# Kernel tuning notes

Hardware: AMD Instinct MI355X
Metric: run time of the kernel (lower is better)

## Reference

```python
import jax, jax.numpy as jnp
import numpy as np

REWARD_SCALE = 1.0
DIST_NORM = 2
LATENT_DIST_THRESHOLD = 6.0

BS, N_VIEWS, N_PART, F_DIM = 128, 4, 1024, 10


def setup_inputs() -> dict:
    key = jax.random.key(0)
    k1, k2, k3, k4 = jax.random.split(key, 4)
    achieved_goal = jax.random.normal(k1, (BS, N_VIEWS, N_PART, F_DIM), jnp.float32)
    desired_goal = jax.random.normal(k2, (BS, N_VIEWS, N_PART, F_DIM), jnp.float32)
    norm_mean = jax.random.normal(k3, (F_DIM,), jnp.float32)
    norm_std = jax.random.uniform(k4, (F_DIM,), jnp.float32, minval=0.5, maxval=1.5)
    return {"achieved_goal": achieved_goal, "desired_goal": desired_goal,
            "norm_mean": norm_mean, "norm_std": norm_std}


def _pairwise_sqdist(x, y):
    # x: [bs, n, d], y: [bs, m, d] -> [bs, n, m] squared L2 ('l2_simple')
    xx = jnp.sum(x * x, axis=-1)            # [bs, n]
    yy = jnp.sum(y * y, axis=-1)            # [bs, m]
    xy = jnp.einsum('bnd,bmd->bnm', x, y)   # [bs, n, m]
    return xx[:, :, None] + yy[:, None, :] - 2.0 * xy


def _particle_mask(particles):
    # latent_classifier is None -> obj_class_cond = ones -> mask = (1 == 0) = all False
    obj_on = particles[..., -1]
    return jnp.zeros_like(obj_on, dtype=bool)


def reference(achieved_goal, desired_goal, norm_mean, norm_std):
    # unnormalize (particle_normalizer.unnormalize modeled as affine)
    state_particles = achieved_goal * norm_std + norm_mean
    goal_particles = desired_goal * norm_std + norm_mean
    bs, n_views, n_particles, _ = state_particles.shape

    state_mask = _particle_mask(state_particles)   # [bs, nv, np] bool
    goal_mask = _particle_mask(goal_particles)

    # P_mask[b,v,i,j] = state_mask[b,v,i] | goal_mask[b,v,j]
    P_mask = jnp.logical_or(state_mask[..., :, None], goal_mask[..., None, :])

    state_vis = state_particles[..., 5:9]
    state_xy = state_particles[..., :2]
    goal_vis = goal_particles[..., 5:9]
    goal_xy = goal_particles[..., :2]

    inf = jnp.asarray(jnp.inf, state_particles.dtype)
    rewards = []
    for i in range(n_views):
        sxy = state_xy[:, i]                 # [bs, np, 2]
        gxy = goal_xy[:, i]
        gmask_i = goal_mask[:, i]            # [bs, np]
        smask_i = state_mask[:, i]

        P = _pairwise_sqdist(state_vis[:, i], goal_vis[:, i])  # [bs, np_state, np_goal]
        P = jnp.where(P_mask[:, i], inf, P)

        # goal -> state direction: min over state dim (axis 1)
        min_d1 = jnp.min(P, axis=1)                            # [bs, np_goal]
        idx1 = jnp.argmin(P, axis=1)                           # [bs, np_goal]
        d_goal = jnp.take_along_axis(sxy, idx1[..., None], axis=1)  # [bs, np_goal, 2]
        xy_dist_1 = jnp.linalg.norm(gxy - d_goal, ord=DIST_NORM, axis=-1)
        xy_dist_1 = jnp.where(min_d1 > LATENT_DIST_THRESHOLD, 1.0, xy_dist_1)
        xy_dist_1 = jnp.where(gmask_i, 0.0, xy_dist_1)
        n_obj_g = jnp.maximum(jnp.sum(~gmask_i, axis=1), 1)
        reward_g2s = -jnp.sum(xy_dist_1, axis=1) / n_obj_g

        # state -> goal direction: min over goal dim (axis 2)
        min_d2 = jnp.min(P, axis=2)
        idx2 = jnp.argmin(P, axis=2)
        d_state = jnp.take_along_axis(gxy, idx2[..., None], axis=1)
        xy_dist_2 = jnp.linalg.norm(sxy - d_state, ord=DIST_NORM, axis=-1)
        xy_dist_2 = jnp.where(min_d2 > LATENT_DIST_THRESHOLD, 1.0, xy_dist_2)
        xy_dist_2 = jnp.where(smask_i, 0.0, xy_dist_2)
        n_obj_s = jnp.maximum(jnp.sum(~smask_i, axis=1), 1)
        reward_s2g = -jnp.sum(xy_dist_2, axis=1) / n_obj_s

        rv = (reward_g2s + reward_s2g) / 2.0
        no_valid = jnp.logical_or(jnp.all(gmask_i, axis=-1), jnp.all(smask_i, axis=-1))
        rv = jnp.where(no_valid, -1.0, rv)
        rewards.append(rv)

    reward = jnp.mean(jnp.stack(rewards, axis=0), axis=0)   # [bs]
    return REWARD_SCALE * reward[:, None]                    # [bs, 1]
```

## Files before the change

kernel.cpp:

```cpp
#include <hip/hip_runtime.h>
#include <cstdint>
#include <cstddef>

#define NP  1024
#define FD  10
#define NV  4
#define BSZ 128
#define TPB 128
#define RPT 8

typedef float v2f __attribute__((ext_vector_type(2)));
typedef float v4f __attribute__((ext_vector_type(4)));

extern "C" __global__ __launch_bounds__(TPB, 2)
void chamfer_pairs(const float* __restrict__ ag, const float* __restrict__ dg,
                   const float* __restrict__ nmean, const float* __restrict__ nstd,
                   float* __restrict__ out )
{
    __shared__ float cxF[NP], cyF[NP], czF[NP], cwF[NP], csF[NP];
    __shared__ float red[TPB / 64];

    const int bid  = blockIdx.x;
    const int pair = bid >> 1;
    const int d    = bid & 1;
    const int tid  = threadIdx.x;

    const float* rowsrc = ((d == 0) ? ag : dg) + (size_t)pair * (NP * FD);
    const float* colsrc = ((d == 0) ? dg : ag) + (size_t)pair * (NP * FD);

    const float s5 = -2.0f * nstd[5], m5 = -2.0f * nmean[5];
    const float s6 = -2.0f * nstd[6], m6 = -2.0f * nmean[6];
    const float s7 = -2.0f * nstd[7], m7 = -2.0f * nmean[7];
    const float s8 = -2.0f * nstd[8], m8 = -2.0f * nmean[8];
    const float std0 = nstd[0], mean0 = nmean[0];
    const float std1 = nstd[1], mean1 = nmean[1];

    for (int m = tid; m < NP; m += TPB) {
        const float* p = colsrc + (size_t)m * FD;
        float t0 = fmaf(p[5], s5, m5);
        float t1 = fmaf(p[6], s6, m6);
        float t2 = fmaf(p[7], s7, m7);
        float t3 = fmaf(p[8], s8, m8);
        cxF[m] = t0; cyF[m] = t1; czF[m] = t2; cwF[m] = t3;
        csF[m] = 0.25f * (t0 * t0 + t1 * t1 + t2 * t2 + t3 * t3);
    }

    float4 rv[RPT];
    float  rthr[RPT];
    float  bestd[RPT];
    int    bblk[RPT];
#pragma unroll
    for (int r = 0; r < RPT; ++r) {
        int n = tid + TPB * r;
        const float* p = rowsrc + (size_t)n * FD;
        float t0 = fmaf(p[5], s5, m5);
        float t1 = fmaf(p[6], s6, m6);
        float t2 = fmaf(p[7], s7, m7);
        float t3 = fmaf(p[8], s8, m8);
        rv[r] = make_float4(-0.5f * t0, -0.5f * t1, -0.5f * t2, -0.5f * t3);
        float rss = 0.25f * (t0 * t0 + t1 * t1 + t2 * t2 + t3 * t3);
        rthr[r] = 6.0f - rss;
        bestd[r] = 3.0e38f;
        bblk[r]  = 0;
    }
    __syncthreads();

    const v4f* X4 = (const v4f*)cxF;
    const v4f* Y4 = (const v4f*)cyF;
    const v4f* Z4 = (const v4f*)czF;
    const v4f* W4 = (const v4f*)cwF;
    const v4f* S4 = (const v4f*)csF;

#pragma unroll 2
    for (int g = 0; g < NP / 8; ++g) {
        const int m = g * 8;
        v4f xA = X4[2 * g], xB = X4[2 * g + 1];
        v4f yA = Y4[2 * g], yB = Y4[2 * g + 1];
        v4f zA = Z4[2 * g], zB = Z4[2 * g + 1];
        v4f wA = W4[2 * g], wB = W4[2 * g + 1];
        v4f cA = S4[2 * g], cB = S4[2 * g + 1];
#pragma unroll
        for (int r = 0; r < RPT; ++r) {
            v2f vx = {rv[r].x, rv[r].x};
            v2f vy = {rv[r].y, rv[r].y};
            v2f vz = {rv[r].z, rv[r].z};
            v2f vw = {rv[r].w, rv[r].w};
            v2f q0 = __builtin_elementwise_fma(vx, xA.lo, cA.lo);
            q0 = __builtin_elementwise_fma(vy, yA.lo, q0);
            q0 = __builtin_elementwise_fma(vz, zA.lo, q0);
            q0 = __builtin_elementwise_fma(vw, wA.lo, q0);
            v2f q1 = __builtin_elementwise_fma(vx, xA.hi, cA.hi);
            q1 = __builtin_elementwise_fma(vy, yA.hi, q1);
            q1 = __builtin_elementwise_fma(vz, zA.hi, q1);
            q1 = __builtin_elementwise_fma(vw, wA.hi, q1);
            v2f q2 = __builtin_elementwise_fma(vx, xB.lo, cB.lo);
            q2 = __builtin_elementwise_fma(vy, yB.lo, q2);
            q2 = __builtin_elementwise_fma(vz, zB.lo, q2);
            q2 = __builtin_elementwise_fma(vw, wB.lo, q2);
            v2f q3 = __builtin_elementwise_fma(vx, xB.hi, cB.hi);
            q3 = __builtin_elementwise_fma(vy, yB.hi, q3);
            q3 = __builtin_elementwise_fma(vz, zB.hi, q3);
            q3 = __builtin_elementwise_fma(vw, wB.hi, q3);
            v2f m01 = __builtin_elementwise_min(q0, q1);
            v2f m23 = __builtin_elementwise_min(q2, q3);
            v2f mm  = __builtin_elementwise_min(m01, m23);
            float bm = fminf(mm.x, mm.y);
            bool lt = bm < bestd[r];
            bestd[r] = fminf(bestd[r], bm);
            bblk[r]  = lt ? m : bblk[r];
        }
    }

    float sum = 0.0f;
#pragma unroll
    for (int r = 0; r < RPT; ++r) {
        int n  = tid + TPB * r;
        int mb = bblk[r];
        float4 v = rv[r];
        float dd[8];
#pragma unroll
        for (int j = 0; j < 8; ++j) {
            float t = fmaf(v.x, cxF[mb + j], csF[mb + j]);
            t = fmaf(v.y, cyF[mb + j], t);
            t = fmaf(v.z, czF[mb + j], t);
            t = fmaf(v.w, cwF[mb + j], t);
            dd[j] = t;
        }
        int sel = 0;
#pragma unroll
        for (int j = 7; j >= 0; --j)
            if (dd[j] == bestd[r]) sel = j;
        int idx = mb + sel;

        float gx = fmaf(colsrc[(size_t)idx * FD + 0], std0, mean0);
        float gy = fmaf(colsrc[(size_t)idx * FD + 1], std1, mean1);
        float ax = fmaf(rowsrc[(size_t)n * FD + 0], std0, mean0);
        float ay = fmaf(rowsrc[(size_t)n * FD + 1], std1, mean1);
        float dx = ax - gx;
        float dy = ay - gy;
        float dist = sqrtf(dx * dx + dy * dy);
        if (bestd[r] > rthr[r]) dist = 1.0f;
        sum += dist;
    }

    for (int o = 32; o > 0; o >>= 1) sum += __shfl_down(sum, o, 64);
    if ((tid & 63) == 0) red[tid >> 6] = sum;
    __syncthreads();
    if (tid == 0) {
        float s = red[0] + red[1];
        atomicAdd(&out[pair >> 2], s * (-1.0f / 8192.0f));
    }
}

extern "C" void kernel_launch(void* const* d_in, const int* in_sizes, int n_in,
                              void* d_out, int out_size, void* d_ws, size_t ws_size,
                              hipStream_t stream)
{
    const float* ag = (const float*)d_in[0];
    const float* dg = (const float*)d_in[1];
    const float* nm = (const float*)d_in[2];
    const float* ns = (const float*)d_in[3];

    hipMemsetAsync(d_out, 0, BSZ * sizeof(float), stream);
    chamfer_pairs<<<BSZ * NV * 2, TPB, 0, stream>>>(ag, dg, nm, ns, (float*)d_out);
}
```

Baseline: 228.2 us.

## Use single-wave blocks with 16 rows per thread and op_sel packed FMAs

Each block is now one 64-thread wave, and each thread handles 16 rows instead of 8. Every shared-memory candidate load is therefore reused across twice as many rows. The inner distance loop uses inline v_pk_fma_f32 with op_sel to broadcast row components, removing the per-row broadcast vector construction. The cross-wave LDS reduction and barrier are dropped, and the argmin refinement recomputes candidate features from global memory. The risk is fewer waves per SIMD to hide latency, plus higher register pressure.

```diff
diff --git a/kernel.cpp b/kernel.cpp
--- a/kernel.cpp
+++ b/kernel.cpp
@@ -4,21 +4,38 @@
 
 #define NP  1024
 #define FD  10
-#define NV  4
 #define BSZ 128
-#define TPB 128
-#define RPT 8
+#define TPB 64
+#define RPT 16
 
 typedef float v2f __attribute__((ext_vector_type(2)));
 typedef float v4f __attribute__((ext_vector_type(4)));
 
-extern "C" __global__ __launch_bounds__(TPB, 2)
+#define SHUF2(v, a, b) __builtin_shufflevector((v), (v), (a), (b))
+
+static __device__ __forceinline__ v2f pk_fma_lo(v2f a, v2f b, v2f c) {
+    v2f d;
+    asm("v_pk_fma_f32 %0, %1, %2, %3 op_sel:[0,0,0] op_sel_hi:[0,1,1]"
+        : "=v"(d) : "v"(a), "v"(b), "v"(c));
+    return d;
+}
+static __device__ __forceinline__ v2f pk_fma_hi(v2f a, v2f b, v2f c) {
+    v2f d;
+    asm("v_pk_fma_f32 %0, %1, %2, %3 op_sel:[1,0,0] op_sel_hi:[1,1,1]"
+        : "=v"(d) : "v"(a), "v"(b), "v"(c));
+    return d;
+}
+
+extern "C" __global__ __launch_bounds__(TPB)
 void chamfer_pairs(const float* __restrict__ ag, const float* __restrict__ dg,
                    const float* __restrict__ nmean, const float* __restrict__ nstd,
                    float* __restrict__ out )
 {
-    __shared__ float cxF[NP], cyF[NP], czF[NP], cwF[NP], csF[NP];
-    __shared__ float red[TPB / 64];
+    __shared__ __align__(16) float cxF[NP];
+    __shared__ __align__(16) float cyF[NP];
+    __shared__ __align__(16) float czF[NP];
+    __shared__ __align__(16) float cwF[NP];
+    __shared__ __align__(16) float csF[NP];
 
     const int bid  = blockIdx.x;
     const int pair = bid >> 1;
@@ -32,6 +49,10 @@
     const float s6 = -2.0f * nstd[6], m6 = -2.0f * nmean[6];
     const float s7 = -2.0f * nstd[7], m7 = -2.0f * nmean[7];
     const float s8 = -2.0f * nstd[8], m8 = -2.0f * nmean[8];
+    const float p5 = nstd[5], q5 = nmean[5];
+    const float p6 = nstd[6], q6 = nmean[6];
+    const float p7 = nstd[7], q7 = nmean[7];
+    const float p8 = nstd[8], q8 = nmean[8];
     const float std0 = nstd[0], mean0 = nmean[0];
     const float std1 = nstd[1], mean1 = nmean[1];
 
@@ -45,21 +66,20 @@
         csF[m] = 0.25f * (t0 * t0 + t1 * t1 + t2 * t2 + t3 * t3);
     }
 
-    float4 rv[RPT];
-    float  rthr[RPT];
-    float  bestd[RPT];
-    int    bblk[RPT];
+    v2f  rxy[RPT];
+    v2f  rzw[RPT];
+    float bestd[RPT];
+    int   bblk[RPT];
 #pragma unroll
     for (int r = 0; r < RPT; ++r) {
         int n = tid + TPB * r;
         const float* p = rowsrc + (size_t)n * FD;
-        float t0 = fmaf(p[5], s5, m5);
-        float t1 = fmaf(p[6], s6, m6);
-        float t2 = fmaf(p[7], s7, m7);
-        float t3 = fmaf(p[8], s8, m8);
-        rv[r] = make_float4(-0.5f * t0, -0.5f * t1, -0.5f * t2, -0.5f * t3);
-        float rss = 0.25f * (t0 * t0 + t1 * t1 + t2 * t2 + t3 * t3);
-        rthr[r] = 6.0f - rss;
+        float a0 = fmaf(p[5], p5, q5);
+        float a1 = fmaf(p[6], p6, q6);
+        float a2 = fmaf(p[7], p7, q7);
+        float a3 = fmaf(p[8], p8, q8);
+        rxy[r].x = a0; rxy[r].y = a1;
+        rzw[r].x = a2; rzw[r].y = a3;
         bestd[r] = 3.0e38f;
         bblk[r]  = 0;
     }
@@ -71,7 +91,6 @@
     const v4f* W4 = (const v4f*)cwF;
     const v4f* S4 = (const v4f*)csF;
 
-#pragma unroll 2
     for (int g = 0; g < NP / 8; ++g) {
         const int m = g * 8;
         v4f xA = X4[2 * g], xB = X4[2 * g + 1];
@@ -79,32 +98,31 @@
         v4f zA = Z4[2 * g], zB = Z4[2 * g + 1];
         v4f wA = W4[2 * g], wB = W4[2 * g + 1];
         v4f cA = S4[2 * g], cB = S4[2 * g + 1];
+        v2f x0 = SHUF2(xA, 0, 1), x1 = SHUF2(xA, 2, 3), x2 = SHUF2(xB, 0, 1), x3 = SHUF2(xB, 2, 3);
+        v2f y0 = SHUF2(yA, 0, 1), y1 = SHUF2(yA, 2, 3), y2 = SHUF2(yB, 0, 1), y3 = SHUF2(yB, 2, 3);
+        v2f z0 = SHUF2(zA, 0, 1), z1 = SHUF2(zA, 2, 3), z2 = SHUF2(zB, 0, 1), z3 = SHUF2(zB, 2, 3);
+        v2f w0 = SHUF2(wA, 0, 1), w1 = SHUF2(wA, 2, 3), w2 = SHUF2(wB, 0, 1), w3 = SHUF2(wB, 2, 3);
+        v2f c0 = SHUF2(cA, 0, 1), c1 = SHUF2(cA, 2, 3), c2 = SHUF2(cB, 0, 1), c3 = SHUF2(cB, 2, 3);
 #pragma unroll
         for (int r = 0; r < RPT; ++r) {
-            v2f vx = {rv[r].x, rv[r].x};
-            v2f vy = {rv[r].y, rv[r].y};
-            v2f vz = {rv[r].z, rv[r].z};
-            v2f vw = {rv[r].w, rv[r].w};
-            v2f q0 = __builtin_elementwise_fma(vx, xA.lo, cA.lo);
-            q0 = __builtin_elementwise_fma(vy, yA.lo, q0);
-            q0 = __builtin_elementwise_fma(vz, zA.lo, q0);
-            q0 = __builtin_elementwise_fma(vw, wA.lo, q0);
-            v2f q1 = __builtin_elementwise_fma(vx, xA.hi, cA.hi);
-            q1 = __builtin_elementwise_fma(vy, yA.hi, q1);
-            q1 = __builtin_elementwise_fma(vz, zA.hi, q1);
-            q1 = __builtin_elementwise_fma(vw, wA.hi, q1);
-            v2f q2 = __builtin_elementwise_fma(vx, xB.lo, cB.lo);
-            q2 = __builtin_elementwise_fma(vy, yB.lo, q2);
-            q2 = __builtin_elementwise_fma(vz, zB.lo, q2);
-            q2 = __builtin_elementwise_fma(vw, wB.lo, q2);
-            v2f q3 = __builtin_elementwise_fma(vx, xB.hi, cB.hi);
-            q3 = __builtin_elementwise_fma(vy, yB.hi, q3);
-            q3 = __builtin_elementwise_fma(vz, zB.hi, q3);
-            q3 = __builtin_elementwise_fma(vw, wB.hi, q3);
-            v2f m01 = __builtin_elementwise_min(q0, q1);
-            v2f m23 = __builtin_elementwise_min(q2, q3);
-            v2f mm  = __builtin_elementwise_min(m01, m23);
-            float bm = fminf(mm.x, mm.y);
+            v2f u0 = pk_fma_lo(rxy[r], x0, c0);
+            u0 = pk_fma_hi(rxy[r], y0, u0);
+            u0 = pk_fma_lo(rzw[r], z0, u0);
+            u0 = pk_fma_hi(rzw[r], w0, u0);
+            v2f u1 = pk_fma_lo(rxy[r], x1, c1);
+            u1 = pk_fma_hi(rxy[r], y1, u1);
+            u1 = pk_fma_lo(rzw[r], z1, u1);
+            u1 = pk_fma_hi(rzw[r], w1, u1);
+            v2f u2 = pk_fma_lo(rxy[r], x2, c2);
+            u2 = pk_fma_hi(rxy[r], y2, u2);
+            u2 = pk_fma_lo(rzw[r], z2, u2);
+            u2 = pk_fma_hi(rzw[r], w2, u2);
+            v2f u3 = pk_fma_lo(rxy[r], x3, c3);
+            u3 = pk_fma_hi(rxy[r], y3, u3);
+            u3 = pk_fma_lo(rzw[r], z3, u3);
+            u3 = pk_fma_hi(rzw[r], w3, u3);
+            float bm = fminf(fminf(fminf(u0.x, u0.y), fminf(u1.x, u1.y)),
+                             fminf(fminf(u2.x, u2.y), fminf(u3.x, u3.y)));
             bool lt = bm < bestd[r];
             bestd[r] = fminf(bestd[r], bm);
             bblk[r]  = lt ? m : bblk[r];
@@ -116,14 +134,20 @@
     for (int r = 0; r < RPT; ++r) {
         int n  = tid + TPB * r;
         int mb = bblk[r];
-        float4 v = rv[r];
+        float vx = rxy[r].x, vy = rxy[r].y, vz = rzw[r].x, vw = rzw[r].y;
         float dd[8];
 #pragma unroll
         for (int j = 0; j < 8; ++j) {
-            float t = fmaf(v.x, cxF[mb + j], csF[mb + j]);
-            t = fmaf(v.y, cyF[mb + j], t);
-            t = fmaf(v.z, czF[mb + j], t);
-            t = fmaf(v.w, cwF[mb + j], t);
+            const float* p = colsrc + (size_t)(mb + j) * FD;
+            float t0 = fmaf(p[5], s5, m5);
+            float t1 = fmaf(p[6], s6, m6);
+            float t2 = fmaf(p[7], s7, m7);
+            float t3 = fmaf(p[8], s8, m8);
+            float cs = 0.25f * (t0 * t0 + t1 * t1 + t2 * t2 + t3 * t3);
+            float t = fmaf(vx, t0, cs);
+            t = fmaf(vy, t1, t);
+            t = fmaf(vz, t2, t);
+            t = fmaf(vw, t3, t);
             dd[j] = t;
         }
         int sel = 0;
@@ -132,23 +156,23 @@
             if (dd[j] == bestd[r]) sel = j;
         int idx = mb + sel;
 
-        float gx = fmaf(colsrc[(size_t)idx * FD + 0], std0, mean0);
-        float gy = fmaf(colsrc[(size_t)idx * FD + 1], std1, mean1);
-        float ax = fmaf(rowsrc[(size_t)n * FD + 0], std0, mean0);
-        float ay = fmaf(rowsrc[(size_t)n * FD + 1], std1, mean1);
+        const float* pc = colsrc + (size_t)idx * FD;
+        float gx = fmaf(pc[0], std0, mean0);
+        float gy = fmaf(pc[1], std1, mean1);
+        const float* pr = rowsrc + (size_t)n * FD;
+        float ax = fmaf(pr[0], std0, mean0);
+        float ay = fmaf(pr[1], std1, mean1);
         float dx = ax - gx;
         float dy = ay - gy;
         float dist = sqrtf(dx * dx + dy * dy);
-        if (bestd[r] > rthr[r]) dist = 1.0f;
+        float rss = vx * vx + vy * vy + vz * vz + vw * vw;
+        if (bestd[r] > 6.0f - rss) dist = 1.0f;
         sum += dist;
     }
 
     for (int o = 32; o > 0; o >>= 1) sum += __shfl_down(sum, o, 64);
-    if ((tid & 63) == 0) red[tid >> 6] = sum;
-    __syncthreads();
     if (tid == 0) {
-        float s = red[0] + red[1];
-        atomicAdd(&out[pair >> 2], s * (-1.0f / 8192.0f));
+        atomicAdd(&out[bid >> 3], sum * (-1.0f / 8192.0f));
     }
 }
 
@@ -162,5 +186,5 @@
     const float* ns = (const float*)d_in[3];
 
     hipMemsetAsync(d_out, 0, BSZ * sizeof(float), stream);
-    chamfer_pairs<<<BSZ * NV * 2, TPB, 0, stream>>>(ag, dg, nm, ns, (float*)d_out);
+    chamfer_pairs<<<BSZ * 4 * 2, TPB, 0, stream>>>(ag, dg, nm, ns, (float*)d_out);
 }
```

Measured after the change: 246.8 us. +8.1%, slower.
